# Optimization experiments

Hardware: AMD Instinct MI355X
Metric: run time of the kernel (lower is better)

## Reference

```python
import jax, jax.numpy as jnp
import numpy as np

B, C, N, H, W = 8, 256, 64, 64, 64
WSCALE = 0.02  # keep energy logits in a sane range


def setup_inputs() -> dict:
    key = jax.random.key(0)
    ks = jax.random.split(key, 8)
    return {
        "X": jax.random.normal(ks[0], (B, C, H, W), dtype=jnp.float32),
        "Wa_w": jax.random.normal(ks[1], (N, C), dtype=jnp.float32) * WSCALE,
        "Wa_b": jnp.zeros((N,), dtype=jnp.float32),
        "Wb_w": jax.random.normal(ks[2], (N, C), dtype=jnp.float32) * WSCALE,
        "Wb_b": jnp.zeros((N,), dtype=jnp.float32),
        "Wg_w": jax.random.normal(ks[3], (N, C), dtype=jnp.float32) * WSCALE,
        "Wg_b": jnp.zeros((N,), dtype=jnp.float32),
        "conv_w": jax.random.normal(ks[4], (C, N), dtype=jnp.float32) * WSCALE,
        "conv_b": jnp.zeros((C,), dtype=jnp.float32),
        "F_w": jax.random.normal(ks[5], (C, C), dtype=jnp.float32) * WSCALE,
        "F_b": jnp.zeros((C,), dtype=jnp.float32),
    }


def reference(X, Wa_w, Wa_b, Wb_w, Wb_b, Wg_w, Wg_b, conv_w, conv_b, F_w, F_b):
    b, c, h, w = X.shape
    L = h * w
    Xf = X.reshape(b, c, L)  # [B,C,L] — 1x1 conv == channel matmul
    alpha = jnp.einsum('nc,bcl->bnl', Wa_w, Xf) + Wa_b[:, None]  # [B,N,L]
    beta = jnp.einsum('nc,bcl->bnl', Wb_w, Xf) + Wb_b[:, None]   # [B,N,L]
    gamma = jnp.einsum('nc,bcl->bnl', Wg_w, Xf) + Wg_b[:, None]  # [B,N,L]
    # energy[b,i,j] = sum_n alpha[b,n,i] * beta[b,n,j]  (alpha^T @ beta)
    energy = jnp.einsum('bni,bnj->bij', alpha, beta)  # [B,L,L]
    attention = jax.nn.softmax(energy, axis=-1)
    # out[b,n,i] = sum_j gamma[b,n,j] * attention[i,j]  (gamma @ attn^T)
    out = jnp.einsum('bnj,bij->bni', gamma, attention)  # [B,N,L]
    out = jnp.einsum('cn,bnl->bcl', conv_w, out) + conv_b[:, None]  # [B,C,L]
    P = jnp.einsum('dc,bcl->bdl', F_w, Xf) + F_b[:, None] + out
    return P.reshape(b, c, h, w)
```

## Files before the change

kernel.cpp:

```cpp
#include <hip/hip_runtime.h>


#define DI __device__ __forceinline__

using f32x4  = __attribute__((ext_vector_type(4))) float;
using bf16x8 = __attribute__((ext_vector_type(8))) short;

static constexpr int B_ = 8, C_ = 256, N_ = 64, L_ = 4096;

DI unsigned short f2bf(float f){
  union{float f; unsigned u;} v; v.f = f;
  unsigned r = (v.u + 0x7FFFu + ((v.u>>16)&1u))>>16;
  return (unsigned short)r;
}
DI float bf2f(unsigned short h){
  union{unsigned u; float f;} v; v.u = ((unsigned)h)<<16; return v.f;
}
DI unsigned pk2(float x, float y){
  return (unsigned)f2bf(x) | ((unsigned)f2bf(y)<<16);
}
DI unsigned swz128(unsigned row, unsigned b){ return row*128u + (b ^ ((row&7u)<<4)); }
DI unsigned swz256(unsigned row, unsigned b){ return row*256u + (b ^ ((row&7u)<<4)); }

DI f32x4 mfma16(bf16x8 a, bf16x8 b, f32x4 c){
  return __builtin_amdgcn_mfma_f32_16x16x32_bf16(a, b, c, 0, 0, 0);
}

__global__ __launch_bounds__(256) void prep_w(
    const float* __restrict__ Wa, const float* __restrict__ Wb,
    const float* __restrict__ Wg, const float* __restrict__ Fw,
    const float* __restrict__ Cw,
    unsigned short* __restrict__ projW, unsigned short* __restrict__ Fhi,
    unsigned short* __restrict__ Flo,  unsigned short* __restrict__ convB){
  int t = blockIdx.x*256 + threadIdx.x;
  int r = t>>8, c = t&255;
  float fv = Fw[t];
  unsigned short h = f2bf(fv);
  Fhi[t] = h;
  Flo[t] = f2bf(fv - bf2f(h));
  if (t < 192*256){
    const float* src = (r<64)? Wa : (r<128)? Wb : Wg;
    projW[t] = f2bf(src[(r&63)*256 + c]);
  }
  if (t < 256*64){
    convB[t] = f2bf(Cw[t]);
  }
}

__global__ __launch_bounds__(256) void prep_x(
    const float* __restrict__ X,
    unsigned short* __restrict__ XhiT, unsigned short* __restrict__ XloT){
  __shared__ float tile[64][65];
  int bid = blockIdx.x;
  int b = bid>>8, cs = (bid>>6)&3, ls = bid&63;
  int t = threadIdx.x;
  int c0 = cs*64, l0 = ls*64;
  const float* Xb = X + ((size_t)b*C_ + c0)*L_ + l0;
  {
    int cc0 = t>>4, l4 = (t&15)*4;
    for (int i=0;i<4;i++){
      int cc = cc0 + 16*i;
      float4 v = *reinterpret_cast<const float4*>(&Xb[(size_t)cc*L_ + l4]);
      tile[cc][l4+0] = v.x; tile[cc][l4+1] = v.y;
      tile[cc][l4+2] = v.z; tile[cc][l4+3] = v.w;
    }
  }
  __syncthreads();
  {
    int c8 = (t&7)*8;
    for (int it=0; it<2; ++it){
      int l = (t>>3) + 32*it;
      float v[8]; unsigned short hs[8], ls8[8];
      for (int e=0;e<8;e++) v[e] = tile[c8+e][l];
      for (int e=0;e<8;e++){
        unsigned short h = f2bf(v[e]);
        hs[e] = h;
        ls8[e] = f2bf(v[e] - bf2f(h));
      }
      uint4 hi, lo;
      hi.x = (unsigned)hs[0] | ((unsigned)hs[1]<<16);
      hi.y = (unsigned)hs[2] | ((unsigned)hs[3]<<16);
      hi.z = (unsigned)hs[4] | ((unsigned)hs[5]<<16);
      hi.w = (unsigned)hs[6] | ((unsigned)hs[7]<<16);
      lo.x = (unsigned)ls8[0] | ((unsigned)ls8[1]<<16);
      lo.y = (unsigned)ls8[2] | ((unsigned)ls8[3]<<16);
      lo.z = (unsigned)ls8[4] | ((unsigned)ls8[5]<<16);
      lo.w = (unsigned)ls8[6] | ((unsigned)ls8[7]<<16);
      size_t o = ((size_t)b*L_ + l0 + l)*C_ + c0 + c8;
      *reinterpret_cast<uint4*>(&XhiT[o]) = hi;
      *reinterpret_cast<uint4*>(&XloT[o]) = lo;
    }
  }
}

__global__ __launch_bounds__(256) void gemm_p(
    const unsigned short* __restrict__ projW, const unsigned short* __restrict__ XhiT,
    const float* __restrict__ Wa_b, const float* __restrict__ Wb_b,
    const float* __restrict__ Wg_b,
    unsigned short* __restrict__ alphaT, unsigned short* __restrict__ betaT,
    unsigned short* __restrict__ gammaV){
  __shared__ alignas(16) char Wl[192*128];
  __shared__ alignas(16) char Xl[64*128];
  __shared__ alignas(16) char tb[64*256];
  int bid = blockIdx.x;
  int b = bid>>6, lt = bid&63, l0 = lt*64;
  int t = threadIdx.x, w = t>>6, lane = t&63;

  f32x4 acc[3][4] = {};
  for (int kc=0; kc<4; kc++){
    {
      int g = t&7; unsigned boff = 16u*g;
      for (int i=0;i<6;i++){
        int row = (t>>3) + 32*i;
        uint4 v = *reinterpret_cast<const uint4*>(&projW[row*256 + kc*64 + g*8]);
        *reinterpret_cast<uint4*>(&Wl[swz128(row, boff)]) = v;
      }
      for (int i=0;i<2;i++){
        int row = (t>>3) + 32*i;
        uint4 v = *reinterpret_cast<const uint4*>(&XhiT[((size_t)b*L_ + l0 + row)*C_ + kc*64 + g*8]);
        *reinterpret_cast<uint4*>(&Xl[swz128(row, boff)]) = v;
      }
    }
    __syncthreads();
    bf16x8 afr[3][2], bfr[4][2];
    for (int mt=0;mt<3;mt++) for (int h=0;h<2;h++){
      int row = 48*w + 16*mt + (lane&15);
      afr[mt][h] = *reinterpret_cast<const bf16x8*>(&Wl[swz128(row, 64u*h + 16u*(lane>>4))]);
    }
    for (int nt=0;nt<4;nt++) for (int h=0;h<2;h++){
      int row = 16*nt + (lane&15);
      bfr[nt][h] = *reinterpret_cast<const bf16x8*>(&Xl[swz128(row, 64u*h + 16u*(lane>>4))]);
    }
    for (int mt=0;mt<3;mt++) for (int nt=0;nt<4;nt++) for (int h=0;h<2;h++)
      acc[mt][nt] = mfma16(afr[mt][h], bfr[nt][h], acc[mt][nt]);
    __syncthreads();
  }
  for (int mt=0;mt<3;mt++){
    int rbase = 48*w + 16*mt;
    for (int q=0;q<4;q++){
      int rg = rbase + 4*(lane>>4) + q;
      float bias = (rg<64)? Wa_b[rg] : (rg<128)? Wb_b[rg-64] : Wg_b[rg-128];
      for (int nt=0;nt<4;nt++){
        float v = acc[mt][nt][q] + bias;
        unsigned short hv = f2bf(v);
        int l = 16*nt + (lane&15);
        if (rg >= 128){
          gammaV[((size_t)b*N_ + (rg-128))*L_ + l0 + l] = hv;
        } else {
          *reinterpret_cast<unsigned short*>(&tb[swz256((unsigned)l, 2u*rg)]) = hv;
        }
      }
    }
  }
  __syncthreads();
  {
    int g8 = t&3, l = t>>2;
    unsigned base = 64u*g8;
    uint4 v0 = *reinterpret_cast<const uint4*>(&tb[swz256((unsigned)l, base)]);
    uint4 v1 = *reinterpret_cast<const uint4*>(&tb[swz256((unsigned)l, base+16u)]);
    uint4 v2 = *reinterpret_cast<const uint4*>(&tb[swz256((unsigned)l, base+32u)]);
    uint4 v3 = *reinterpret_cast<const uint4*>(&tb[swz256((unsigned)l, base+48u)]);
    int half = (g8<2)? g8 : g8-2;
    unsigned short* dst = (g8<2) ? &alphaT[((size_t)b*L_ + l0 + l)*N_ + 32*half]
                                 : &betaT [((size_t)b*L_ + l0 + l)*N_ + 32*half];
    *reinterpret_cast<uint4*>(dst)    = v0;
    *reinterpret_cast<uint4*>(dst+8)  = v1;
    *reinterpret_cast<uint4*>(dst+16) = v2;
    *reinterpret_cast<uint4*>(dst+24) = v3;
  }
}

__global__ __launch_bounds__(256) void gemm_f(
    const unsigned short* __restrict__ Fhi, const unsigned short* __restrict__ Flo,
    const unsigned short* __restrict__ XhiT, const unsigned short* __restrict__ XloT,
    float* __restrict__ FX){
  __shared__ alignas(16) char Fh[256*80], Fl[256*80];
  __shared__ alignas(16) char Xh[64*80],  Xlo[64*80];
  int bid = blockIdx.x; int b = bid>>6, lt = bid&63, l0 = lt*64;
  int t = threadIdx.x, w = t>>6, lane = t&63;
  f32x4 acc[4][4] = {};
  for (int kc=0; kc<8; kc++){
    int g = t&3; unsigned boff = 16u*g;
    for (int i=0;i<4;i++){
      int row = (t>>2) + 64*i;
      *reinterpret_cast<uint4*>(&Fh[row*80u + boff]) =
        *reinterpret_cast<const uint4*>(&Fhi[row*256 + kc*32 + g*8]);
      *reinterpret_cast<uint4*>(&Fl[row*80u + boff]) =
        *reinterpret_cast<const uint4*>(&Flo[row*256 + kc*32 + g*8]);
    }
    {
      int row = t>>2;
      *reinterpret_cast<uint4*>(&Xh[row*80u + boff]) =
        *reinterpret_cast<const uint4*>(&XhiT[((size_t)b*L_ + l0 + row)*C_ + kc*32 + g*8]);
      *reinterpret_cast<uint4*>(&Xlo[row*80u + boff]) =
        *reinterpret_cast<const uint4*>(&XloT[((size_t)b*L_ + l0 + row)*C_ + kc*32 + g*8]);
    }
    __syncthreads();
    bf16x8 ah[4], al[4], bh[4], bl[4];
    for (int mt=0;mt<4;mt++){
      int row = 64*w + 16*mt + (lane&15);
      unsigned off = row*80u + 16u*(lane>>4);
      ah[mt] = *reinterpret_cast<const bf16x8*>(&Fh[off]);
      al[mt] = *reinterpret_cast<const bf16x8*>(&Fl[off]);
    }
    for (int nt=0;nt<4;nt++){
      int row = 16*nt + (lane&15);
      unsigned off = row*80u + 16u*(lane>>4);
      bh[nt] = *reinterpret_cast<const bf16x8*>(&Xh[off]);
      bl[nt] = *reinterpret_cast<const bf16x8*>(&Xlo[off]);
    }
    for (int mt=0;mt<4;mt++) for (int nt=0;nt<4;nt++){
      acc[mt][nt] = mfma16(ah[mt], bh[nt], acc[mt][nt]);
      acc[mt][nt] = mfma16(ah[mt], bl[nt], acc[mt][nt]);
      acc[mt][nt] = mfma16(al[mt], bh[nt], acc[mt][nt]);
    }
    __syncthreads();
  }
  for (int mt=0;mt<4;mt++) for (int q=0;q<4;q++){
    int c = 64*w + 16*mt + 4*(lane>>4) + q;
    for (int nt=0;nt<4;nt++){
      int l = l0 + 16*nt + (lane&15);
      FX[((size_t)b*C_ + c)*L_ + l] = acc[mt][nt][q];
    }
  }
}

__global__ __launch_bounds__(256) void attn(
    const unsigned short* __restrict__ alphaT, const unsigned short* __restrict__ betaT,
    const unsigned short* __restrict__ gammaV,
    float* __restrict__ Opart, float* __restrict__ lpart){
  __shared__ alignas(16) char smem[40960];
  const unsigned QS = 0u, KS0 = 8192u, VS0 = 24576u, PS = 0u;
  int orig = blockIdx.x;
  int bid = ((orig&7)<<7) | (orig>>3);
  int b = bid>>7, qt = (bid>>1)&63, half = bid&1;
  int i0 = qt*64, kvb = half*2048;
  int t = threadIdx.x, w = t>>6, lane = t&63;
  int g = t&7; unsigned boff = 16u*g;
  int srow = t>>3;

  {
    for (int i=0;i<2;i++){
      int row = srow + 32*i;
      *reinterpret_cast<uint4*>(&smem[QS + swz128(row,boff)]) =
        *reinterpret_cast<const uint4*>(&alphaT[((size_t)b*L_ + i0 + row)*N_ + g*8]);
      *reinterpret_cast<uint4*>(&smem[KS0 + swz128(row,boff)]) =
        *reinterpret_cast<const uint4*>(&betaT[((size_t)b*L_ + kvb + row)*N_ + g*8]);
      *reinterpret_cast<uint4*>(&smem[VS0 + swz128(row,boff)]) =
        *reinterpret_cast<const uint4*>(&gammaV[((size_t)b*N_ + row)*L_ + kvb + g*8]);
    }
  }
  __syncthreads();
  bf16x8 qa[2];
  for (int h=0;h<2;h++){
    int row = 16*w + (lane&15);
    qa[h] = *reinterpret_cast<const bf16x8*>(&smem[QS + swz128(row, 64u*h + 16u*(lane>>4))]);
  }
  __syncthreads();
  f32x4 accO[4] = {};
  float l_run[4] = {0.f, 0.f, 0.f, 0.f};

  for (int kt=0; kt<32; kt++){
    unsigned kb  = KS0 + (unsigned)(kt&1)*8192u;
    unsigned vb  = VS0 + (unsigned)(kt&1)*8192u;
    unsigned kb1 = KS0 + (unsigned)((kt+1)&1)*8192u;
    unsigned vb1 = VS0 + (unsigned)((kt+1)&1)*8192u;
    uint4 kreg0 = {}, kreg1 = {}, vreg0 = {}, vreg1 = {};
    if (kt < 31){
      int kv0 = kvb + (kt+1)*64;
      kreg0 = *reinterpret_cast<const uint4*>(&betaT[((size_t)b*L_ + kv0 + srow)*N_ + g*8]);
      kreg1 = *reinterpret_cast<const uint4*>(&betaT[((size_t)b*L_ + kv0 + srow+32)*N_ + g*8]);
      vreg0 = *reinterpret_cast<const uint4*>(&gammaV[((size_t)b*N_ + srow)*L_ + kv0 + g*8]);
      vreg1 = *reinterpret_cast<const uint4*>(&gammaV[((size_t)b*N_ + srow+32)*L_ + kv0 + g*8]);
    }
    f32x4 accS[4] = {};
    for (int nt=0;nt<4;nt++){
      for (int h=0;h<2;h++){
        int row = 16*nt + (lane&15);
        bf16x8 kfr = *reinterpret_cast<const bf16x8*>(&smem[kb + swz128(row, 64u*h + 16u*(lane>>4))]);
        accS[nt] = mfma16(qa[h], kfr, accS[nt]);
      }
    }
    for (int nt=0;nt<4;nt++){
      for (int q=0;q<4;q++){
        float p = __expf(accS[nt][q]);
        l_run[q] += p;
        int prow = 16*w + 4*(lane>>4) + q;
        int pcol = 16*nt + (lane&15);
        *reinterpret_cast<unsigned short*>(&smem[PS + swz128((unsigned)prow, 2u*pcol)]) = f2bf(p);
      }
    }
    for (int h=0;h<2;h++){
      int prow = 16*w + (lane&15);
      bf16x8 pa = *reinterpret_cast<const bf16x8*>(&smem[PS + swz128((unsigned)prow, 64u*h + 16u*(lane>>4))]);
      for (int dt=0;dt<4;dt++){
        int row = 16*dt + (lane&15);
        bf16x8 vfr = *reinterpret_cast<const bf16x8*>(&smem[vb + swz128(row, 64u*h + 16u*(lane>>4))]);
        accO[dt] = mfma16(pa, vfr, accO[dt]);
      }
    }
    if (kt < 31){
      *reinterpret_cast<uint4*>(&smem[kb1 + swz128((unsigned)srow, boff)])      = kreg0;
      *reinterpret_cast<uint4*>(&smem[kb1 + swz128((unsigned)(srow+32), boff)]) = kreg1;
      *reinterpret_cast<uint4*>(&smem[vb1 + swz128((unsigned)srow, boff)])      = vreg0;
      *reinterpret_cast<uint4*>(&smem[vb1 + swz128((unsigned)(srow+32), boff)]) = vreg1;
    }
    __syncthreads();
  }
  for (int m=1;m<16;m<<=1)
    for (int q=0;q<4;q++) l_run[q] += __shfl_xor(l_run[q], m);
  size_t obase = (size_t)bid * 4096;
  for (int dt=0;dt<4;dt++){
    for (int q=0;q<4;q++){
      int i = 16*w + 4*(lane>>4) + q;
      int d = 16*dt + (lane&15);
      Opart[obase + i*64 + d] = accO[dt][q];
    }
  }
  if ((lane&15)==0){
    for (int q=0;q<4;q++){
      int i = 16*w + 4*(lane>>4) + q;
      lpart[((size_t)b*2 + half)*L_ + i0 + i] = l_run[q];
    }
  }
}

__global__ __launch_bounds__(256) void combine(
    const float* __restrict__ Opart, const float* __restrict__ lpart,
    const unsigned short* __restrict__ convB,
    const float* __restrict__ F_b, const float* __restrict__ conv_b,
    float* __restrict__ Out){
  __shared__ alignas(16) char Os[8192];
  __shared__ alignas(16) char Cs[32768];
  __shared__ float linv[64];
  int bid = blockIdx.x;
  int b = bid>>6, qt = bid&63, i0 = qt*64;
  int t = threadIdx.x, w = t>>6, lane = t&63;
  int g = t&7; unsigned boff = 16u*g; int srow = t>>3;
  for (int i=0;i<8;i++){
    int row = srow + 32*i;
    *reinterpret_cast<uint4*>(&Cs[swz128(row,boff)]) =
      *reinterpret_cast<const uint4*>(&convB[row*64 + g*8]);
  }
  if (t < 64){
    float l0 = lpart[(size_t)(b*2+0)*L_ + i0 + t];
    float l1 = lpart[(size_t)(b*2+1)*L_ + i0 + t];
    linv[t] = 1.f/(l0+l1);
  }
  __syncthreads();
  {
    int i = t>>2, c4 = t&3;
    float inv = linv[i];
    size_t base0 = ((size_t)(b*64+qt)*2)*4096 + i*64 + c4*16;
    size_t base1 = base0 + 4096;
    float4 a0 = *reinterpret_cast<const float4*>(&Opart[base0]);
    float4 a1 = *reinterpret_cast<const float4*>(&Opart[base0+4]);
    float4 a2 = *reinterpret_cast<const float4*>(&Opart[base0+8]);
    float4 a3 = *reinterpret_cast<const float4*>(&Opart[base0+12]);
    float4 b0 = *reinterpret_cast<const float4*>(&Opart[base1]);
    float4 b1 = *reinterpret_cast<const float4*>(&Opart[base1+4]);
    float4 b2 = *reinterpret_cast<const float4*>(&Opart[base1+8]);
    float4 b3 = *reinterpret_cast<const float4*>(&Opart[base1+12]);
    uint4 w0, w1;
    w0.x = pk2((a0.x+b0.x)*inv, (a0.y+b0.y)*inv);
    w0.y = pk2((a0.z+b0.z)*inv, (a0.w+b0.w)*inv);
    w0.z = pk2((a1.x+b1.x)*inv, (a1.y+b1.y)*inv);
    w0.w = pk2((a1.z+b1.z)*inv, (a1.w+b1.w)*inv);
    w1.x = pk2((a2.x+b2.x)*inv, (a2.y+b2.y)*inv);
    w1.y = pk2((a2.z+b2.z)*inv, (a2.w+b2.w)*inv);
    w1.z = pk2((a3.x+b3.x)*inv, (a3.y+b3.y)*inv);
    w1.w = pk2((a3.z+b3.z)*inv, (a3.w+b3.w)*inv);
    *reinterpret_cast<uint4*>(&Os[swz128((unsigned)i, 32u*c4)])      = w0;
    *reinterpret_cast<uint4*>(&Os[swz128((unsigned)i, 32u*c4+16u)])  = w1;
  }
  __syncthreads();
  bf16x8 ob[4][2];
  for (int it=0;it<4;it++) for (int h=0;h<2;h++){
    int row = 16*it + (lane&15);
    ob[it][h] = *reinterpret_cast<const bf16x8*>(&Os[swz128(row, 64u*h + 16u*(lane>>4))]);
  }
  for (int ct=0;ct<4;ct++){
    bf16x8 ca[2];
    for (int h=0;h<2;h++){
      int row = 64*w + 16*ct + (lane&15);
      ca[h] = *reinterpret_cast<const bf16x8*>(&Cs[swz128(row, 64u*h + 16u*(lane>>4))]);
    }
    for (int it=0;it<4;it++){
      f32x4 accC = {};
      for (int h=0;h<2;h++) accC = mfma16(ca[h], ob[it][h], accC);
      for (int q=0;q<4;q++){
        int c = 64*w + 16*ct + 4*(lane>>4) + q;
        int l = i0 + 16*it + (lane&15);
        size_t o = ((size_t)b*C_ + c)*L_ + l;
        Out[o] = Out[o] + accC[q] + F_b[c] + conv_b[c];
      }
    }
  }
}

extern "C" void kernel_launch(void* const* d_in, const int* in_sizes, int n_in,
                              void* d_out, int out_size, void* d_ws, size_t ws_size,
                              hipStream_t stream){
  const float* X     = (const float*)d_in[0];
  const float* Wa_w  = (const float*)d_in[1];
  const float* Wa_b  = (const float*)d_in[2];
  const float* Wb_w  = (const float*)d_in[3];
  const float* Wb_b  = (const float*)d_in[4];
  const float* Wg_w  = (const float*)d_in[5];
  const float* Wg_b  = (const float*)d_in[6];
  const float* conv_w= (const float*)d_in[7];
  const float* conv_b= (const float*)d_in[8];
  const float* F_w   = (const float*)d_in[9];
  const float* F_b   = (const float*)d_in[10];

  const size_t WS_NEEDED = 46530560;
  if (ws_size < WS_NEEDED) return;

  char* ws = (char*)d_ws;
  unsigned short* XhiT   = (unsigned short*)(ws);
  unsigned short* XloT   = (unsigned short*)(ws + 16777216);
  unsigned short* alphaT = (unsigned short*)(ws + 33554432);
  unsigned short* betaT  = (unsigned short*)(ws + 37748736);
  unsigned short* gammaV = (unsigned short*)(ws + 41943040);
  unsigned short* projW  = (unsigned short*)(ws + 46137344);
  unsigned short* Fhi    = (unsigned short*)(ws + 46235648);
  unsigned short* Flo    = (unsigned short*)(ws + 46366720);
  unsigned short* convB  = (unsigned short*)(ws + 46497792);
  float* lpart = (float*)(ws);
  float* Opart = (float*)(ws + 16777216);
  float* Out = (float*)d_out;

  hipLaunchKernelGGL(prep_w, dim3(256), dim3(256), 0, stream,
                     Wa_w, Wb_w, Wg_w, F_w, conv_w, projW, Fhi, Flo, convB);
  hipLaunchKernelGGL(prep_x, dim3(2048), dim3(256), 0, stream, X, XhiT, XloT);
  hipLaunchKernelGGL(gemm_p, dim3(512), dim3(256), 0, stream,
                     projW, XhiT, Wa_b, Wb_b, Wg_b, alphaT, betaT, gammaV);
  hipLaunchKernelGGL(gemm_f, dim3(512), dim3(256), 0, stream,
                     Fhi, Flo, XhiT, XloT, Out);
  hipLaunchKernelGGL(attn, dim3(1024), dim3(256), 0, stream,
                     alphaT, betaT, gammaV, Opart, lpart);
  hipLaunchKernelGGL(combine, dim3(512), dim3(256), 0, stream,
                     Opart, lpart, convB, F_b, conv_b, Out);
}
```

Measured before the change: 217.9 us.

## Transpose QK MFMA, fold log2e into beta weights, use exp2 and packed bf16 P stores

Folds log2(e) into the beta projection weights and bias so the softmax can use exp2 directly instead of __expf. Swaps the MFMA operands for the score tile so each lane holds four consecutive key columns of one query row. This lets the probabilities be packed with v_cvt_pk_bf16_f32 into one 8-byte LDS store instead of four scalar 2-byte stores, and it reduces the row-sum to a single accumulator with two shuffles. It adds bf16 rounding of the log2e-scaled beta and relies on inline asm for the pack conversion.

```diff
diff --git a/kernel.cpp b/kernel.cpp
--- a/kernel.cpp
+++ b/kernel.cpp
@@ -7,6 +7,7 @@
 using bf16x8 = __attribute__((ext_vector_type(8))) short;
 
 static constexpr int B_ = 8, C_ = 256, N_ = 64, L_ = 4096;
+static constexpr float LOG2E = 1.44269504088896340736f;
 
 DI unsigned short f2bf(float f){
   union{float f; unsigned u;} v; v.f = f;
@@ -40,7 +41,8 @@
   Flo[t] = f2bf(fv - bf2f(h));
   if (t < 192*256){
     const float* src = (r<64)? Wa : (r<128)? Wb : Wg;
-    projW[t] = f2bf(src[(r&63)*256 + c]);
+    float s = (r>=64 && r<128) ? LOG2E : 1.f;
+    projW[t] = f2bf(src[(r&63)*256 + c] * s);
   }
   if (t < 256*64){
     convB[t] = f2bf(Cw[t]);
@@ -139,7 +141,7 @@
     int rbase = 48*w + 16*mt;
     for (int q=0;q<4;q++){
       int rg = rbase + 4*(lane>>4) + q;
-      float bias = (rg<64)? Wa_b[rg] : (rg<128)? Wb_b[rg-64] : Wg_b[rg-128];
+      float bias = (rg<64)? Wa_b[rg] : (rg<128)? Wb_b[rg-64]*LOG2E : Wg_b[rg-128];
       for (int nt=0;nt<4;nt++){
         float v = acc[mt][nt][q] + bias;
         unsigned short hv = f2bf(v);
@@ -258,7 +260,9 @@
   }
   __syncthreads();
   f32x4 accO[4] = {};
-  float l_run[4] = {0.f, 0.f, 0.f, 0.f};
+  float l_run = 0.f;
+  unsigned prow = 16u*(unsigned)w + (unsigned)(lane&15);
+  unsigned lg = (unsigned)(lane>>4);
 
   for (int kt=0; kt<32; kt++){
     unsigned kb  = KS0 + (unsigned)(kt&1)*8192u;
@@ -278,21 +282,26 @@
       for (int h=0;h<2;h++){
         int row = 16*nt + (lane&15);
         bf16x8 kfr = *reinterpret_cast<const bf16x8*>(&smem[kb + swz128(row, 64u*h + 16u*(lane>>4))]);
-        accS[nt] = mfma16(qa[h], kfr, accS[nt]);
+        accS[nt] = mfma16(kfr, qa[h], accS[nt]);
       }
     }
     for (int nt=0;nt<4;nt++){
-      for (int q=0;q<4;q++){
-        float p = __expf(accS[nt][q]);
-        l_run[q] += p;
-        int prow = 16*w + 4*(lane>>4) + q;
-        int pcol = 16*nt + (lane&15);
-        *reinterpret_cast<unsigned short*>(&smem[PS + swz128((unsigned)prow, 2u*pcol)]) = f2bf(p);
-      }
+      float p0 = exp2f(accS[nt][0]);
+      float p1 = exp2f(accS[nt][1]);
+      float p2 = exp2f(accS[nt][2]);
+      float p3 = exp2f(accS[nt][3]);
+      l_run += (p0+p1)+(p2+p3);
+      unsigned w0, w1;
+      asm("v_cvt_pk_bf16_f32 %0, %1, %2" : "=v"(w0) : "v"(p0), "v"(p1));
+      asm("v_cvt_pk_bf16_f32 %0, %1, %2" : "=v"(w1) : "v"(p2), "v"(p3));
+      unsigned bcol = 32u*(unsigned)nt + 8u*lg;
+      unsigned addr = swz128(prow, bcol & ~15u) + (bcol & 8u);
+      uint2 pv; pv.x = w0; pv.y = w1;
+      *reinterpret_cast<uint2*>(&smem[PS + addr]) = pv;
     }
     for (int h=0;h<2;h++){
-      int prow = 16*w + (lane&15);
-      bf16x8 pa = *reinterpret_cast<const bf16x8*>(&smem[PS + swz128((unsigned)prow, 64u*h + 16u*(lane>>4))]);
+      int pr = 16*w + (lane&15);
+      bf16x8 pa = *reinterpret_cast<const bf16x8*>(&smem[PS + swz128((unsigned)pr, 64u*h + 16u*(lane>>4))]);
       for (int dt=0;dt<4;dt++){
         int row = 16*dt + (lane&15);
         bf16x8 vfr = *reinterpret_cast<const bf16x8*>(&smem[vb + swz128(row, 64u*h + 16u*(lane>>4))]);
@@ -307,8 +316,8 @@
     }
     __syncthreads();
   }
-  for (int m=1;m<16;m<<=1)
-    for (int q=0;q<4;q++) l_run[q] += __shfl_xor(l_run[q], m);
+  l_run += __shfl_xor(l_run, 16);
+  l_run += __shfl_xor(l_run, 32);
   size_t obase = (size_t)bid * 4096;
   for (int dt=0;dt<4;dt++){
     for (int q=0;q<4;q++){
@@ -317,11 +326,8 @@
       Opart[obase + i*64 + d] = accO[dt][q];
     }
   }
-  if ((lane&15)==0){
-    for (int q=0;q<4;q++){
-      int i = 16*w + 4*(lane>>4) + q;
-      lpart[((size_t)b*2 + half)*L_ + i0 + i] = l_run[q];
-    }
+  if (lane < 16){
+    lpart[((size_t)b*2 + half)*L_ + i0 + 16*w + lane] = l_run;
   }
 }
 
```

Result: slower. 223.1 us (+2.4%).
